# Performance work log

Measured on AMD Instinct MI355X. Metric: run time of the kernel, lower is better.

Reference implementation:

```python
import jax, jax.numpy as jnp
import numpy as np

N = 30000; E = 480000; B = 60
IN = 200; ID = 128; H = 128
NEXP = 4; TOPK = 2; TEMP = 1.5
HEADS = 4; DH = H // HEADS


def _ln(x, g, b):
    mu = jnp.mean(x, -1, keepdims=True)
    var = jnp.var(x, -1, keepdims=True)
    return (x - mu) / jnp.sqrt(var + 1e-5) * g + b


def _seg_sum(d, i, n):
    return jax.ops.segment_sum(d, i, num_segments=n)


def setup_inputs():
    key = jax.random.key(0)
    kit = iter(jax.random.split(key, 80))
    def w(*s):
        return jax.random.normal(next(kit), s, jnp.float32) * 0.05
    inp = {}
    inp['x'] = jax.random.normal(next(kit), (N, IN), jnp.float32)
    inp['node_identity'] = jax.random.normal(next(kit), (N, ID), jnp.float32)
    inp['edge_index'] = jax.random.randint(next(kit), (2, E), 0, N)
    inp['batch'] = jnp.sort(jax.random.randint(next(kit), (N,), 0, B))
    inp.update(fe_W=w(IN, H), fe_b=jnp.zeros(H), fe_g=jnp.ones(H), fe_be=jnp.zeros(H))
    inp.update(ie_W=w(ID, H), ie_b=jnp.zeros(H), ie_g=jnp.ones(H), ie_be=jnp.zeros(H))
    inp.update(fuse_W=w(2 * H, H), fuse_b=jnp.zeros(H), fuse_g=jnp.ones(H), fuse_be=jnp.zeros(H))
    inp.update(router_W=w(2 * H, NEXP))
    inp.update(mlp_W1=w(H, H), mlp_b1=jnp.zeros(H), mlp_W2=w(H, H), mlp_b2=jnp.zeros(H))
    inp.update(cheb_W=w(2, 2, H, H), cheb_b=jnp.zeros((2, H)))
    inp.update(gt_Wq=w(2, H, H), gt_bq=jnp.zeros((2, H)), gt_Wk=w(2, H, H), gt_bk=jnp.zeros((2, H)),
               gt_Wv=w(2, H, H), gt_bv=jnp.zeros((2, H)), gt_Ws=w(2, H, H), gt_bs=jnp.zeros((2, H)))
    inp.update(gcn_W=w(2, H, H), gcn_b=jnp.zeros((2, H)))
    inp.update(pn_g=jnp.ones((NEXP, H)), pn_b=jnp.zeros((NEXP, H)), expert_scales=jnp.ones(NEXP))
    inp.update(h1_W=w(H, H), h1_b=jnp.zeros(H), h1_g=jnp.ones(H), h1_be=jnp.zeros(H))
    inp.update(h2_W=w(H, H // 2), h2_b=jnp.zeros(H // 2), h2_g=jnp.ones(H // 2), h2_be=jnp.zeros(H // 2))
    inp.update(h3_W=w(H // 2, 2), h3_b=jnp.zeros(2), logit_bias=jnp.zeros(2))
    return inp


def _forward(x, node_identity, edge_index, batch, fe_W, fe_b, fe_g, fe_be, ie_W, ie_b, ie_g, ie_be,
             fuse_W, fuse_b, fuse_g, fuse_be, router_W, mlp_W1, mlp_b1, mlp_W2, mlp_b2, cheb_W, cheb_b,
             gt_Wq, gt_bq, gt_Wk, gt_bk, gt_Wv, gt_bv, gt_Ws, gt_bs, gcn_W, gcn_b, pn_g, pn_b,
             expert_scales, h1_W, h1_b, h1_g, h1_be, h2_W, h2_b, h2_g, h2_be, h3_W, h3_b, logit_bias):
    relu = jax.nn.relu
    src, dst = edge_index[0], edge_index[1]
    # encoders + fuse
    h_x = relu(_ln(x @ fe_W + fe_b, fe_g, fe_be))
    h_id = relu(_ln(node_identity @ ie_W + ie_b, ie_g, ie_be))
    h_router = jnp.concatenate([h_x, h_id], -1)
    h = relu(_ln(h_router @ fuse_W + fuse_b, fuse_g, fuse_be))
    # noisy top-k router (eval: no noise, no dropout)
    node_logits = h_router @ router_W
    probs = jax.nn.softmax(node_logits / TEMP, -1)
    vals, idx = jax.lax.top_k(probs, TOPK)
    wts = vals / jnp.clip(jnp.sum(vals, -1, keepdims=True), 1e-9)
    gates = jnp.zeros_like(probs).at[jnp.arange(N)[:, None], idx].set(wts)  # [N, 4]
    # degree / normalization terms
    ones_e = jnp.ones(E, jnp.float32)
    deg = _seg_sum(ones_e, dst, N)
    dinv = jnp.where(deg > 0, jax.lax.rsqrt(jnp.maximum(deg, 1.0)), 0.0)
    dinvl = jax.lax.rsqrt(deg + 1.0)  # with self loops (GCN)
    enorm = dinv[src] * dinv[dst]
    enorml = dinvl[src] * dinvl[dst]
    def aprop(xx, en, di_self=None):
        out = _seg_sum(xx[src] * en[:, None], dst, N)
        if di_self is not None:
            out = out + xx * di_self[:, None]
        return out
    # Expert 0: MLP (2 layers)
    e0 = relu(h @ mlp_W1 + mlp_b1) @ mlp_W2 + mlp_b2
    # Expert 1: ChebNet K=2 (lambda_max=2 -> L_hat = -A_norm), 2 layers
    z = h
    for l in range(2):
        tx1 = -aprop(z, enorm)
        z = z @ cheb_W[l, 0] + tx1 @ cheb_W[l, 1] + cheb_b[l]
        if l == 0:
            z = relu(z)
    e1 = z
    # Expert 2: Graph Transformer, 2 layers, heads=4, root-weight skip
    z = h
    for l in range(2):
        q = (z @ gt_Wq[l] + gt_bq[l]).reshape(N, HEADS, DH)
        k = (z @ gt_Wk[l] + gt_bk[l]).reshape(N, HEADS, DH)
        v = (z @ gt_Wv[l] + gt_bv[l]).reshape(N, HEADS, DH)
        logits = jnp.sum(q[dst] * k[src], -1) * (1.0 / DH ** 0.5)  # [E, heads]
        m = jax.ops.segment_max(logits, dst, num_segments=N)
        m = jnp.where(jnp.isfinite(m), m, 0.0)
        p = jnp.exp(logits - m[dst])
        denom = jnp.clip(_seg_sum(p, dst, N), 1e-9)
        attn = p / denom[dst]
        agg = _seg_sum(attn[:, :, None] * v[src], dst, N).reshape(N, H)
        z = agg + z @ gt_Ws[l] + gt_bs[l]
        if l == 0:
            z = relu(z)
    e2 = z
    # Expert 3: GCN, 2 layers, self loops
    z = h
    for l in range(2):
        zw = z @ gcn_W[l]
        z = aprop(zw, enorml, dinvl * dinvl) + gcn_b[l]
        if l == 0:
            z = relu(z)
    e3 = z
    # per-expert post-norm, scale, gated combine + residual
    eo = jnp.stack([e0, e1, e2, e3], 0)  # [4, N, H]
    eo = _ln(eo, pn_g[:, None, :], pn_b[:, None, :]) * expert_scales[:, None, None]
    out = h + jnp.einsum('ne,enh->nh', gates, eo)
    # mean-pool readout per graph
    counts = jnp.clip(_seg_sum(jnp.ones(N, jnp.float32), batch, B), 1.0)
    pooled = _seg_sum(out, batch, B) / counts[:, None]
    # classification head
    zc = relu(_ln(pooled @ h1_W + h1_b, h1_g, h1_be))
    zc = relu(_ln(zc @ h2_W + h2_b, h2_g, h2_be))
    return zc @ h3_W + h3_b + logit_bias


def reference(x, node_identity, edge_index, batch, fe_W, fe_b, fe_g, fe_be, ie_W, ie_b, ie_g, ie_be,
              fuse_W, fuse_b, fuse_g, fuse_be, router_W, mlp_W1, mlp_b1, mlp_W2, mlp_b2, cheb_W, cheb_b,
              gt_Wq, gt_bq, gt_Wk, gt_bk, gt_Wv, gt_bv, gt_Ws, gt_bs, gcn_W, gcn_b, pn_g, pn_b,
              expert_scales, h1_W, h1_b, h1_g, h1_be, h2_W, h2_b, h2_g, h2_be, h3_W, h3_b, logit_bias):
    return _forward(x, node_identity, edge_index, batch, fe_W, fe_b, fe_g, fe_be, ie_W, ie_b, ie_g, ie_be,
                    fuse_W, fuse_b, fuse_g, fuse_be, router_W, mlp_W1, mlp_b1, mlp_W2, mlp_b2, cheb_W, cheb_b,
                    gt_Wq, gt_bq, gt_Wk, gt_bk, gt_Wv, gt_bv, gt_Ws, gt_bs, gcn_W, gcn_b, pn_g, pn_b,
                    expert_scales, h1_W, h1_b, h1_g, h1_be, h2_W, h2_b, h2_g, h2_be, h3_W, h3_b, logit_bias)
```

## Files before the change

### kernel.cpp

```cpp
#include <hip/hip_runtime.h>

#define RELUF 1
#define ACCF  2
#define LNF   4
#define PCH   32
#define NWT   19
#define SCH   2048

typedef unsigned short ushort_t;
typedef __attribute__((ext_vector_type(8))) short bf16x8;
typedef __attribute__((ext_vector_type(4))) float f32x4;

__device__ __forceinline__ float bf2f(unsigned int v) {
    return __uint_as_float(v << 16);
}
__device__ __forceinline__ unsigned int f2bu(float f) {
    unsigned int u = __float_as_uint(f);
    return (u + 0x7fffu + ((u >> 16) & 1u)) >> 16;
}
__device__ __forceinline__ void unpack8(uint4 u, float* f) {
    f[0] = bf2f(u.x & 0xffff); f[1] = bf2f(u.x >> 16);
    f[2] = bf2f(u.y & 0xffff); f[3] = bf2f(u.y >> 16);
    f[4] = bf2f(u.z & 0xffff); f[5] = bf2f(u.z >> 16);
    f[6] = bf2f(u.w & 0xffff); f[7] = bf2f(u.w >> 16);
// ... 99 lines not shown
        dinvl[i] = rsqrtf(deg + 1.f);
    }
}

struct WtPack {
    const float* src[NWT];
    unsigned long long off[NWT];
    int K[NWT];
};
__global__ void wconv_kernel(WtPack p, ushort_t* __restrict__ base) {
    int a = blockIdx.y;
    const float* s = p.src[a];
    ushort_t* d = base + p.off[a];
    int K = p.K[a];
    int total = K * 128;
    for (int i = blockIdx.x * blockDim.x + threadIdx.x; i < total; i += gridDim.x * blockDim.x) {
        int k = i >> 7, n = i & 127;
        d[n * K + k] = (ushort_t)f2bu(s[i]);
    }
}

__global__ __launch_bounds__(256)
void gemm_f32_ln_kernel(const float* __restrict__ A, int lda, int K,
                        const ushort_t* __restrict__ Wt,
                        ushort_t* __restrict__ Cb,
                        int M,
                        const float* __restrict__ bias,
                        const float* __restrict__ g, const float* __restrict__ be,
                        const float* __restrict__ rW,
                        float* __restrict__ logits)
{
    __shared__ ushort_t As[64][40];
    __shared__ ushort_t Bs[128][40];
    const int tid = threadIdx.x;
    const int m0 = blockIdx.x * 64;
    const int lane = tid & 63;
    const int wv = tid >> 6;
    const int q = lane >> 4;
    const int l16 = lane & 15;
    const int sar = tid >> 2;
    const int sak = (tid & 3) << 3;
    const int sbn = tid >> 1;
    const int sbk = (tid & 1) << 4;
    const bool arow_ok = (m0 + sar) < M;
    const float* Arow = A + (size_t)(m0 + sar) * lda;
    const ushort_t* Wrow = Wt + (size_t)sbn * K;

    f32x4 acc[8];
#pragma unroll
    for (int t = 0; t < 8; t++) acc[t] = (f32x4){0.f, 0.f, 0.f, 0.f};

    for (int k0 = 0; k0 < K; k0 += 32) {
        uint4 apk;
        if (arow_ok && k0 + sak + 8 <= K) {
            float4 p0 = *(const float4*)(Arow + k0 + sak);
            float4 p1 = *(const float4*)(Arow + k0 + sak + 4);
            apk.x = f2bu(p0.x) | (f2bu(p0.y) << 16);
            apk.y = f2bu(p0.z) | (f2bu(p0.w) << 16);
            apk.z = f2bu(p1.x) | (f2bu(p1.y) << 16);
            apk.w = f2bu(p1.z) | (f2bu(p1.w) << 16);
        } else {
            unsigned int t4[4] = {0, 0, 0, 0};
            for (int j = 0; j < 8; j++) {
                int k = k0 + sak + j;
                unsigned int bv = (arow_ok && k < K) ? f2bu(Arow[k]) : 0u;
                t4[j >> 1] |= bv << ((j & 1) * 16);
            }
            apk = make_uint4(t4[0], t4[1], t4[2], t4[3]);
        }
        uint4 b0, b1;
        if (k0 + sbk + 16 <= K) {
            b0 = *(const uint4*)(Wrow + k0 + sbk);
            b1 = *(const uint4*)(Wrow + k0 + sbk + 8);
        } else {
            unsigned int t8[8] = {0, 0, 0, 0, 0, 0, 0, 0};
            for (int j = 0; j < 16; j++) {
                int k = k0 + sbk + j;
                unsigned int bv = (k < K) ? (unsigned int)Wrow[k] : 0u;
                t8[j >> 1] |= bv << ((j & 1) * 16);
            }
            b0 = make_uint4(t8[0], t8[1], t8[2], t8[3]);
            b1 = make_uint4(t8[4], t8[5], t8[6], t8[7]);
        }
        __syncthreads();
        *(uint4*)&As[sar][sak] = apk;
        *(uint4*)&Bs[sbn][sbk] = b0;
        *(uint4*)&Bs[sbn][sbk + 8] = b1;
        __syncthreads();
        bf16x8 af = *(const bf16x8*)&As[16 * wv + l16][q * 8];
#pragma unroll
        for (int t = 0; t < 8; t++) {
            bf16x8 bf = *(const bf16x8*)&Bs[t * 16 + l16][q * 8];
            acc[t] = __builtin_amdgcn_mfma_f32_16x16x32_bf16(af, bf, acc[t], 0, 0, 0);
        }
    }
    const int row_base = m0 + 16 * wv + q * 4;
#pragma unroll
    for (int t = 0; t < 8; t++) {
        float bb = bias[t * 16 + l16];
#pragma unroll
        for (int r = 0; r < 4; r++) acc[t][r] += bb;
    }
    float mean[4], inv[4];
#pragma unroll
    for (int r = 0; r < 4; r++) {
        float s = 0.f, sq = 0.f;
#pragma unroll
        for (int t = 0; t < 8; t++) { float v = acc[t][r]; s += v; sq = fmaf(v, v, sq); }
#pragma unroll
        for (int off = 1; off <= 8; off <<= 1) { s += __shfl_xor(s, off); sq += __shfl_xor(sq, off); }
        mean[r] = s * (1.f / 128.f);
        float var = sq * (1.f / 128.f) - mean[r] * mean[r];
        inv[r] = rsqrtf(var + 1e-5f);
    }
    float rl0[4] = {0, 0, 0, 0}, rl1[4] = {0, 0, 0, 0};
    float rl2[4] = {0, 0, 0, 0}, rl3[4] = {0, 0, 0, 0};
#pragma unroll
    for (int t = 0; t < 8; t++) {
        int col = t * 16 + l16;
        float gg = g[col], b2 = be[col];
        float4 rw = *(const float4*)(rW + col * 4);
#pragma unroll
        for (int r = 0; r < 4; r++) {
            float y = fmaxf(fmaf((acc[t][r] - mean[r]) * inv[r], gg, b2), 0.f);
            rl0[r] = fmaf(y, rw.x, rl0[r]);
            rl1[r] = fmaf(y, rw.y, rl1[r]);
            rl2[r] = fmaf(y, rw.z, rl2[r]);
            rl3[r] = fmaf(y, rw.w, rl3[r]);
            float other = __shfl_xor(y, 1);
            int row = row_base + r;
            if (!(l16 & 1) && row < M) {
                unsigned int pk = f2bu(y) | (f2bu(other) << 16);
                *(unsigned int*)(Cb + (size_t)row * 256 + col) = pk;
            }
        }
    }
#pragma unroll
    for (int r = 0; r < 4; r++) {
#pragma unroll
        for (int off = 1; off <= 8; off <<= 1) {
            rl0[r] += __shfl_xor(rl0[r], off);
            rl1[r] += __shfl_xor(rl1[r], off);
            rl2[r] += __shfl_xor(rl2[r], off);
            rl3[r] += __shfl_xor(rl3[r], off);
        }
        int row = row_base + r;
        if (l16 == 0 && row < M)
            *(float4*)(logits + (size_t)row * 4) = make_float4(rl0[r], rl1[r], rl2[r], rl3[r]);
    }
}

template <int K>
__global__ __launch_bounds__(256)
void gemm_bf_kernel(const ushort_t* __restrict__ A,
                    const ushort_t* __restrict__ Wt,
                    ushort_t* __restrict__ Cb,
                    int M, const float* __restrict__ bias, int flags,
                    const float* __restrict__ g, const float* __restrict__ be)
{
    __shared__ ushort_t As[64][40];
    __shared__ ushort_t Bs[128][40];
    const int tid = threadIdx.x;
    const int m0 = blockIdx.x * 64;
    const int lane = tid & 63;
    const int wv = tid >> 6;
    const int q = lane >> 4;
    const int l16 = lane & 15;
    const int sar = tid >> 2;
    const int sak = (tid & 3) << 3;
    const int sbn = tid >> 1;
    const int sbk = (tid & 1) << 4;
    const bool arow_ok = (m0 + sar) < M;
    const ushort_t* Arow = A + (size_t)(m0 + sar) * K;
    const ushort_t* Wrow = Wt + (size_t)sbn * K;

    f32x4 acc[8];
#pragma unroll
    for (int t = 0; t < 8; t++) acc[t] = (f32x4){0.f, 0.f, 0.f, 0.f};

#pragma unroll
    for (int k0 = 0; k0 < K; k0 += 32) {
        uint4 apk = arow_ok ? *(const uint4*)(Arow + k0 + sak) : make_uint4(0, 0, 0, 0);
        uint4 b0 = *(const uint4*)(Wrow + k0 + sbk);
        uint4 b1 = *(const uint4*)(Wrow + k0 + sbk + 8);
        __syncthreads();
        *(uint4*)&As[sar][sak] = apk;
        *(uint4*)&Bs[sbn][sbk] = b0;
        *(uint4*)&Bs[sbn][sbk + 8] = b1;
        __syncthreads();
        bf16x8 af = *(const bf16x8*)&As[16 * wv + l16][q * 8];
#pragma unroll
        for (int t = 0; t < 8; t++) {
            bf16x8 bf = *(const bf16x8*)&Bs[t * 16 + l16][q * 8];
            acc[t] = __builtin_amdgcn_mfma_f32_16x16x32_bf16(af, bf, acc[t], 0, 0, 0);
        }
    }
    const int row_base = m0 + 16 * wv + q * 4;
    if (flags & LNF) {
#pragma unroll
        for (int t = 0; t < 8; t++) {
            float bb = bias[t * 16 + l16];
#pragma unroll
            for (int r = 0; r < 4; r++) acc[t][r] += bb;
        }
        float mean[4], inv[4];
#pragma unroll
        for (int r = 0; r < 4; r++) {
            float s = 0.f, sq = 0.f;
#pragma unroll
            for (int t = 0; t < 8; t++) { float v = acc[t][r]; s += v; sq = fmaf(v, v, sq); }
#pragma unroll
            for (int off = 1; off <= 8; off <<= 1) { s += __shfl_xor(s, off); sq += __shfl_xor(sq, off); }
            mean[r] = s * (1.f / 128.f);
            float var = sq * (1.f / 128.f) - mean[r] * mean[r];
            inv[r] = rsqrtf(var + 1e-5f);
        }
#pragma unroll
        for (int t = 0; t < 8; t++) {
            int col = t * 16 + l16;
            float gg = g[col], b2 = be[col];
#pragma unroll
            for (int r = 0; r < 4; r++) {
                float y = fmaf((acc[t][r] - mean[r]) * inv[r], gg, b2);
                if (flags & RELUF) y = fmaxf(y, 0.f);
                float other = __shfl_xor(y, 1);
                int row = row_base + r;
                if (!(l16 & 1) && row < M) {
                    unsigned int pk = f2bu(y) | (f2bu(other) << 16);
                    *(unsigned int*)(Cb + (size_t)row * 128 + col) = pk;
                }
            }
        }
        return;
    }
#pragma unroll
    for (int t = 0; t < 8; t++) {
        int col = t * 16 + l16;
        float bb = bias ? bias[col] : 0.f;
#pragma unroll
        for (int r = 0; r < 4; r++) {
            int row = row_base + r;
            bool ok = row < M;
            float val = acc[t][r] + bb;
            if ((flags & ACCF) && ok) val += bf2f(Cb[(size_t)row * 128 + col]);
            if (flags & RELUF) val = fmaxf(val, 0.f);
            float other = __shfl_xor(val, 1);
            if (!(lane & 1) && ok) {
                unsigned int pk = f2bu(val) | (f2bu(other) << 16);
                *(unsigned int*)(Cb + (size_t)row * 128 + col) = pk;
            }
        }
    }
}

__global__ __launch_bounds__(256)
void gemm_dual_kernel(const ushort_t* __restrict__ A1, const ushort_t* __restrict__ Wt1,
                      const ushort_t* __restrict__ A2, const ushort_t* __restrict__ Wt2,
                      ushort_t* __restrict__ Cb, int M,
                      const float* __restrict__ bias, int flags)
{
    const int K = 128;
    __shared__ ushort_t As[64][40];
    __shared__ ushort_t Bs[128][40];
    const int tid = threadIdx.x;
    const int m0 = blockIdx.x * 64;
    const int lane = tid & 63;
    const int wv = tid >> 6;
    const int q = lane >> 4;
    const int l16 = lane & 15;
    const int sar = tid >> 2;
    const int sak = (tid & 3) << 3;
    const int sbn = tid >> 1;
    const int sbk = (tid & 1) << 4;
    const bool arow_ok = (m0 + sar) < M;

    f32x4 acc[8];
#pragma unroll
    for (int t = 0; t < 8; t++) acc[t] = (f32x4){0.f, 0.f, 0.f, 0.f};

    for (int ph = 0; ph < 2; ph++) {
        const ushort_t* Arow = (ph ? A2 : A1) + (size_t)(m0 + sar) * K;
        const ushort_t* Wrow = (ph ? Wt2 : Wt1) + (size_t)sbn * K;
        for (int k0 = 0; k0 < K; k0 += 32) {
            uint4 apk = arow_ok ? *(const uint4*)(Arow + k0 + sak) : make_uint4(0, 0, 0, 0);
            uint4 b0 = *(const uint4*)(Wrow + k0 + sbk);
            uint4 b1 = *(const uint4*)(Wrow + k0 + sbk + 8);
            __syncthreads();
            *(uint4*)&As[sar][sak] = apk;
            *(uint4*)&Bs[sbn][sbk] = b0;
            *(uint4*)&Bs[sbn][sbk + 8] = b1;
            __syncthreads();
            bf16x8 af = *(const bf16x8*)&As[16 * wv + l16][q * 8];
#pragma unroll
            for (int t = 0; t < 8; t++) {
                bf16x8 bf = *(const bf16x8*)&Bs[t * 16 + l16][q * 8];
                acc[t] = __builtin_amdgcn_mfma_f32_16x16x32_bf16(af, bf, acc[t], 0, 0, 0);
            }
        }
    }
#pragma unroll
    for (int t = 0; t < 8; t++) {
        int col = t * 16 + l16;
        float bb = bias ? bias[col] : 0.f;
#pragma unroll
        for (int r = 0; r < 4; r++) {
            int row = m0 + 16 * wv + q * 4 + r;
            bool ok = row < M;
            float val = acc[t][r] + bb;
            if (flags & RELUF) val = fmaxf(val, 0.f);
            float other = __shfl_xor(val, 1);
            if (!(lane & 1) && ok) {
                unsigned int pk = f2bu(val) | (f2bu(other) << 16);
                *(unsigned int*)(Cb + (size_t)row * 128 + col) = pk;
            }
        }
    }
}

__global__ __launch_bounds__(256)
void gemm4_kernel(const ushort_t* __restrict__ A,
                  const ushort_t* __restrict__ Wt,
                  ushort_t* __restrict__ qb,
                  ushort_t* __restrict__ kv,
                  ushort_t* __restrict__ sk,
                  int M,
                  const float* __restrict__ b0, const float* __restrict__ b1,
                  const float* __restrict__ b2, const float* __restrict__ b3)
{
    const int K = 128;
    __shared__ ushort_t As[64][40];
    __shared__ ushort_t Bs[512][40];
    const int tid = threadIdx.x;
    const int m0 = blockIdx.x * 64;
    const int lane = tid & 63;
    const int wv = tid >> 6;
    const int q = lane >> 4;
    const int l16 = lane & 15;
    const int sar = tid >> 2;
    const int sak = (tid & 3) << 3;
    const bool arow_ok = (m0 + sar) < M;
    const ushort_t* Arow = A + (size_t)(m0 + sar) * K;

    f32x4 acc[32];
#pragma unroll
    for (int t = 0; t < 32; t++) acc[t] = (f32x4){0.f, 0.f, 0.f, 0.f};

    for (int k0 = 0; k0 < K; k0 += 32) {
        uint4 apk = arow_ok ? *(const uint4*)(Arow + k0 + sak) : make_uint4(0, 0, 0, 0);
        uint4 bv[4][2];
        int rows[4], kofs[4];
#pragma unroll
        for (int j = 0; j < 4; j++) {
            int slot = tid + j * 256;
            rows[j] = slot >> 1;
            kofs[j] = (slot & 1) << 4;
            const ushort_t* Wrow = Wt + (size_t)rows[j] * K + k0 + kofs[j];
            bv[j][0] = *(const uint4*)Wrow;
            bv[j][1] = *(const uint4*)(Wrow + 8);
        }
        __syncthreads();
        *(uint4*)&As[sar][sak] = apk;
#pragma unroll
        for (int j = 0; j < 4; j++) {
            *(uint4*)&Bs[rows[j]][kofs[j]] = bv[j][0];
            *(uint4*)&Bs[rows[j]][kofs[j] + 8] = bv[j][1];
        }
        __syncthreads();
        bf16x8 af = *(const bf16x8*)&As[16 * wv + l16][q * 8];
#pragma unroll
        for (int t = 0; t < 32; t++) {
            bf16x8 bf = *(const bf16x8*)&Bs[t * 16 + l16][q * 8];
            acc[t] = __builtin_amdgcn_mfma_f32_16x16x32_bf16(af, bf, acc[t], 0, 0, 0);
        }
    }
    const float* bs4[4] = {b0, b1, b2, b3};
#pragma unroll
    for (int s = 0; s < 4; s++) {
#pragma unroll
        for (int t8 = 0; t8 < 8; t8++) {
            int t = s * 8 + t8;
            int col = t8 * 16 + l16;
            float bb = bs4[s][col];
#pragma unroll
            for (int r = 0; r < 4; r++) {
                int row = m0 + 16 * wv + q * 4 + r;
                bool ok = row < M;
                float val = acc[t][r] + bb;
                float other = __shfl_xor(val, 1);
                if (!(lane & 1) && ok) {
                    unsigned int pk = f2bu(val) | (f2bu(other) << 16);
                    if (s == 0)
                        *(unsigned int*)(qb + (size_t)row * 128 + col) = pk;
                    else if (s == 3)
                        *(unsigned int*)(sk + (size_t)row * 128 + col) = pk;
                    else
                        *(unsigned int*)(kv + (size_t)row * 256 + (s - 1) * 128 + col) = pk;
                }
            }
        }
    }
}

__global__ void topk_kernel(const float* __restrict__ la, const float* __restrict__ lb,
                            float* __restrict__ gates, int M)
{
    int n = blockIdx.x * blockDim.x + threadIdx.x;
    if (n >= M) return;
    float4 a = *(const float4*)(la + (size_t)n * 4);
    float4 b = *(const float4*)(lb + (size_t)n * 4);
    float l[4] = {(a.x + b.x) * (1.f / 1.5f), (a.y + b.y) * (1.f / 1.5f),
                  (a.z + b.z) * (1.f / 1.5f), (a.w + b.w) * (1.f / 1.5f)};
    float mx = fmaxf(fmaxf(l[0], l[1]), fmaxf(l[2], l[3]));
    float e[4], ssum = 0.f;
#pragma unroll
    for (int i = 0; i < 4; i++) { e[i] = expf(l[i] - mx); ssum += e[i]; }
    float p[4];
#pragma unroll
    for (int i = 0; i < 4; i++) p[i] = e[i] / ssum;
    int i0 = 0;
    for (int i = 1; i < 4; i++) if (p[i] > p[i0]) i0 = i;
    int i1 = -1;
    for (int i = 0; i < 4; i++) {
        if (i == i0) continue;
        if (i1 < 0 || p[i] > p[i1]) i1 = i;
    }
    float wsum = fmaxf(p[i0] + p[i1], 1e-9f);
    float gg[4] = {0.f, 0.f, 0.f, 0.f};
    gg[i0] = p[i0] / wsum;
    gg[i1] = p[i1] / wsum;
    *(float4*)(gates + (size_t)n * 4) = make_float4(gg[0], gg[1], gg[2], gg[3]);
}

__global__ void edge_deg_kernel(const int* __restrict__ dst, int* __restrict__ degi, int E) {
    int e = blockIdx.x * blockDim.x + threadIdx.x;
    if (e < E) atomicAdd(&degi[dst[e]], 1);
}
__global__ void csr_fill_kernel(const int* __restrict__ src, const int* __restrict__ dst,
                                const int* __restrict__ rowptr, int* __restrict__ cursor,
                                int* __restrict__ csr,
                                const float* __restrict__ dinv, const float* __restrict__ dinvl,
                                float* __restrict__ ecA, float* __restrict__ ecB, int E) {
    int e = blockIdx.x * blockDim.x + threadIdx.x;
    if (e >= E) return;
    int d = dst[e];
    int s = src[e];
    int pos = atomicAdd(&cursor[d], 1);
    int o = rowptr[d] + pos;
    csr[o] = s;
    ecA[o] = dinv[d] * dinv[s];
    ecB[o] = dinvl[d] * dinvl[s];
}

__global__ void gather2_kernel(const ushort_t* __restrict__ Xb,
                               ushort_t* __restrict__ OutA, ushort_t* __restrict__ OutB,
                               const int* __restrict__ rowptr, const int* __restrict__ csr,
                               const float* __restrict__ ecA, const float* __restrict__ ecB,
                               const float* __restrict__ dinvl, int M)
{
    int node = blockIdx.x * 4 + (threadIdx.x >> 6);
    int lane = threadIdx.x & 63;
    if (node >= M) return;
    int beg = rowptr[node], end = rowptr[node + 1];
    int slot = lane >> 4, g = lane & 15;
    float aA[8] = {0, 0, 0, 0, 0, 0, 0, 0};
    float aB[8] = {0, 0, 0, 0, 0, 0, 0, 0};
    int s0 = 0, s1 = 0;
    float cA0 = 0.f, cB0 = 0.f, cA1 = 0.f, cB1 = 0.f;
    {
        int r0 = beg + slot, r1 = beg + 4 + slot;
        if (r0 < end) { s0 = csr[r0]; cA0 = ecA[r0]; cB0 = ecB[r0]; }
        if (r1 < end) { s1 = csr[r1]; cA1 = ecA[r1]; cB1 = ecB[r1]; }
    }
    for (int e = beg; e < end; e += 8) {
        int ns0 = 0, ns1 = 0;
        float nA0 = 0.f, nB0 = 0.f, nA1 = 0.f, nB1 = 0.f;
        int nr0 = e + 8 + slot, nr1 = e + 12 + slot;
        if (nr0 < end) { ns0 = csr[nr0]; nA0 = ecA[nr0]; nB0 = ecB[nr0]; }
        if (nr1 < end) { ns1 = csr[nr1]; nA1 = ecA[nr1]; nB1 = ecB[nr1]; }
        uint4 x0 = *(const uint4*)(Xb + (size_t)s0 * 128 + g * 8);
        uint4 x1 = *(const uint4*)(Xb + (size_t)s1 * 128 + g * 8);
        fma8(x0, cA0, aA); fma8(x0, cB0, aB);
        fma8(x1, cA1, aA); fma8(x1, cB1, aB);
        s0 = ns0; s1 = ns1;
        cA0 = nA0; cB0 = nB0; cA1 = nA1; cB1 = nB1;
    }
#pragma unroll
    for (int j = 0; j < 8; j++) {
        aA[j] += __shfl_xor(aA[j], 16); aA[j] += __shfl_xor(aA[j], 32);
        aB[j] += __shfl_xor(aB[j], 16); aB[j] += __shfl_xor(aB[j], 32);
    }
    {
        float c = dinvl[node]; c *= c;
        uint4 xs = *(const uint4*)(Xb + (size_t)node * 128 + g * 8);
        fma8(xs, c, aB);
    }
    if (lane < 16) {
        float oA[8], oB[8];
#pragma unroll
        for (int j = 0; j < 8; j++) { oA[j] = -aA[j]; oB[j] = aB[j]; }
        size_t ofs = (size_t)node * 128 + g * 8;
        *(uint4*)(OutA + ofs) = pack8(oA);
        *(uint4*)(OutB + ofs) = pack8(oB);
    }
}

__global__ void gather_l2_kernel(const ushort_t* __restrict__ XA, const ushort_t* __restrict__ XB,
                                 ushort_t* __restrict__ OutA, ushort_t* __restrict__ OutB,
                                 const int* __restrict__ rowptr, const int* __restrict__ csr,
                                 const float* __restrict__ ecA, const float* __restrict__ ecB,
                                 const float* __restrict__ dinvl, int M)
{
    int node = blockIdx.x * 4 + (threadIdx.x >> 6);
    int lane = threadIdx.x & 63;
    if (node >= M) return;
    int beg = rowptr[node], end = rowptr[node + 1];
    int slot = lane >> 4, g = lane & 15;
    float aA[8] = {0, 0, 0, 0, 0, 0, 0, 0};
    float aB[8] = {0, 0, 0, 0, 0, 0, 0, 0};
    int s0 = 0, s1 = 0;
    float cA0 = 0.f, cB0 = 0.f, cA1 = 0.f, cB1 = 0.f;
    {
        int r0 = beg + slot, r1 = beg + 4 + slot;
        if (r0 < end) { s0 = csr[r0]; cA0 = ecA[r0]; cB0 = ecB[r0]; }
        if (r1 < end) { s1 = csr[r1]; cA1 = ecA[r1]; cB1 = ecB[r1]; }
    }
    for (int e = beg; e < end; e += 8) {
        int ns0 = 0, ns1 = 0;
        float nA0 = 0.f, nB0 = 0.f, nA1 = 0.f, nB1 = 0.f;
        int nr0 = e + 8 + slot, nr1 = e + 12 + slot;
        if (nr0 < end) { ns0 = csr[nr0]; nA0 = ecA[nr0]; nB0 = ecB[nr0]; }
        if (nr1 < end) { ns1 = csr[nr1]; nA1 = ecA[nr1]; nB1 = ecB[nr1]; }
        uint4 a0 = *(const uint4*)(XA + (size_t)s0 * 128 + g * 8);
        uint4 a1 = *(const uint4*)(XA + (size_t)s1 * 128 + g * 8);
        uint4 b0 = *(const uint4*)(XB + (size_t)s0 * 128 + g * 8);
        uint4 b1 = *(const uint4*)(XB + (size_t)s1 * 128 + g * 8);
        fma8(a0, cA0, aA); fma8(a1, cA1, aA);
        fma8(b0, cB0, aB); fma8(b1, cB1, aB);
        s0 = ns0; s1 = ns1;
        cA0 = nA0; cB0 = nB0; cA1 = nA1; cB1 = nB1;
    }
#pragma unroll
    for (int j = 0; j < 8; j++) {
        aA[j] += __shfl_xor(aA[j], 16); aA[j] += __shfl_xor(aA[j], 32);
        aB[j] += __shfl_xor(aB[j], 16); aB[j] += __shfl_xor(aB[j], 32);
    }
    {
        float c = dinvl[node]; c *= c;
        uint4 xs = *(const uint4*)(XB + (size_t)node * 128 + g * 8);
        fma8(xs, c, aB);
    }
// ... 88 lines not shown
        ba[ee] = pnb[ee * 128 + lane * 2];
        bb[ee] = pnb[ee * 128 + lane * 2 + 1];
        es[ee] = esc[ee];
    }
    float sx = 0.f, sy = 0.f;
    for (int n = s0 + c; n < e0i; n += PCH) {
        size_t ofs = (size_t)n * 128 + lane * 2;
        float4 gg = *(const float4*)(gates + (size_t)n * 4);
        float gv[4] = {gg.x, gg.y, gg.z, gg.w};
        unsigned int hu = *(const unsigned int*)(hb + ofs);
        float ox = bf2f(hu & 0xffff), oy = bf2f(hu >> 16);
#pragma unroll
        for (int ee = 0; ee < 4; ee++) {
            unsigned int u = *(const unsigned int*)(eps[ee] + ofs);
            float vx = bf2f(u & 0xffff), vy = bf2f(u >> 16);
            float su = vx + vy, sq = vx * vx + vy * vy;
#pragma unroll
            for (int off = 32; off; off >>= 1) { su += __shfl_xor(su, off); sq += __shfl_xor(sq, off); }
            float mean = su * (1.f / 128.f);
            float var = sq * (1.f / 128.f) - mean * mean;
            float inv = rsqrtf(var + 1e-5f);
            float cc = es[ee] * gv[ee];
            ox = fmaf(cc, (vx - mean) * inv * ga[ee] + ba[ee], ox);
            oy = fmaf(cc, (vy - mean) * inv * gb[ee] + bb[ee], oy);
        }
        sx += ox; sy += oy;
    }
    *(float2*)(partial + ((size_t)b * PCH + c) * 128 + lane * 2) = make_float2(sx, sy);
}

__global__ void head_kernel(const float* __restrict__ partial,
                            const int* __restrict__ bstart, const int* __restrict__ bend,
                            const float* __restrict__ h1W, const float* __restrict__ h1b,
                            const float* __restrict__ h1g, const float* __restrict__ h1be,
                            const float* __restrict__ h2W, const float* __restrict__ h2b,
                            const float* __restrict__ h2g, const float* __restrict__ h2be,
                            const float* __restrict__ h3W, const float* __restrict__ h3b,
                            const float* __restrict__ lbias,
                            float* __restrict__ out, int B)
{
    __shared__ float p[128], z[128];
    int b = blockIdx.x, t = threadIdx.x;
    float sum = 0.f;
#pragma unroll
    for (int c = 0; c < PCH; c++) sum += partial[((size_t)b * PCH + c) * 128 + t];
    float cnt = fmaxf((float)(bend[b] - bstart[b]), 1.f);
    p[t] = sum / cnt;
    __syncthreads();
    float a = h1b[t];
    for (int k = 0; k < 128; k++) a = fmaf(p[k], h1W[k * 128 + t], a);
    z[t] = a;
    __syncthreads();
    float s = 0.f, sq = 0.f;
    for (int k = 0; k < 128; k++) { float x = z[k]; s += x; sq += x * x; }
    float mean = s * (1.f / 128.f), var = sq * (1.f / 128.f) - mean * mean;
    float y = fmaxf((a - mean) * rsqrtf(var + 1e-5f) * h1g[t] + h1be[t], 0.f);
    __syncthreads();
    z[t] = y;
    __syncthreads();
    float a2 = 0.f;
    if (t < 64) {
        a2 = h2b[t];
        for (int k = 0; k < 128; k++) a2 = fmaf(z[k], h2W[k * 64 + t], a2);
    }
    __syncthreads();
    if (t < 64) p[t] = a2;
    __syncthreads();
    if (t < 2) {
        float s2 = 0.f, sq2 = 0.f;
        for (int k = 0; k < 64; k++) { float x = p[k]; s2 += x; sq2 += x * x; }
        float mean2 = s2 * (1.f / 64.f), var2 = sq2 * (1.f / 64.f) - mean2 * mean2;
        float inv2 = rsqrtf(var2 + 1e-5f);
        float o = h3b[t] + lbias[t];
        for (int k = 0; k < 64; k++) {
            float zc = fmaxf((p[k] - mean2) * inv2 * h2g[k] + h2be[k], 0.f);
            o = fmaf(zc, h3W[k * 2 + t], o);
        }
        out[b * 2 + t] = o;
    }
}

extern "C" void kernel_launch(void* const* d_in, const int* in_sizes, int n_in,
                              void* d_out, int out_size, void* d_ws, size_t ws_size,
                              hipStream_t stream)
{
    (void)ws_size; (void)n_in;
    const int N = in_sizes[3];
    const int E = in_sizes[2] / 2;
    const int B = out_size / 2;

    const int* ei = (const int*)d_in[2];
    const int* src = ei;
    const int* dst = ei + E;
    const int* batch = (const int*)d_in[3];

    const float* W[47];
    for (int i = 0; i < 47; i++) W[i] = (const float*)d_in[i];

    size_t fN = (size_t)N;
    float* gates   = (float*)d_ws;
    float* dinv    = gates + 4 * fN;
    float* dinvl   = dinv + fN;
    float* partial = dinvl + fN;
    float* logitsA = partial + (size_t)128 * B * PCH;
    float* logitsB = logitsA + 4 * fN;
    ushort_t* hb  = (ushort_t*)(logitsB + 4 * fN);
    ushort_t* e0b = hb + 128 * fN;
    ushort_t* e1b = e0b + 128 * fN;
    ushort_t* e2b = e1b + 128 * fN;
    ushort_t* e3b = e2b + 128 * fN;
    ushort_t* x0  = e3b + 128 * fN;
    ushort_t* x1  = x0 + 128 * fN;
    ushort_t* x2  = x1 + 128 * fN;
    ushort_t* x3  = x2 + 128 * fN;
    ushort_t* qb  = x3 + 128 * fN;
    ushort_t* kvb = qb + 128 * fN;
    ushort_t* hrb = kvb + 256 * fN;
    ushort_t* wt  = hrb + 256 * fN;
    WtPack wp;
    const float* wsrc[NWT] = {
        W[4], W[8], W[12], W[17], W[19],
        W[21], W[21] + 16384, W[21] + 32768, W[21] + 49152,
        W[23], W[25], W[27], W[29],
        W[23] + 16384, W[25] + 16384, W[27] + 16384, W[29] + 16384,
        W[31], W[31] + 16384
    };
    const int wk[NWT] = {200, 128, 256, 128, 128,
                         128, 128, 128, 128,
                         128, 128, 128, 128,
                         128, 128, 128, 128,
                         128, 128};
    unsigned long long woff[NWT];
    unsigned long long acc_off = 0;
    for (int i = 0; i < NWT; i++) {
        wp.src[i] = wsrc[i];
        wp.K[i] = wk[i];
        wp.off[i] = acc_off;
        woff[i] = acc_off;
        acc_off += (unsigned long long)128 * wk[i];
    }
    int* degi   = (int*)(wt + acc_off + 8);
    int* cursor = degi + N;
    int* rowptr = cursor + N;
    int* csr    = rowptr + (N + 1);
    int* bstart = csr + E;
    int* bend   = bstart + B;
    int* bsum   = bend + B;
    float* ecA  = (float*)(bsum + 256);
    float* ecB  = ecA + E;

    dim3 blk(256);
    int gN4 = (N + 3) / 4;
    dim3 gG((N + 63) / 64);
    int nsb = (N + SCH - 1) / SCH;

    wconv_kernel<<<dim3(32, NWT), blk, 0, stream>>>(wp, wt);
    zero2_kernel<<<(2 * N + 255) / 256, blk, 0, stream>>>(degi, 2 * N, bstart, 2 * B);
    seg_bounds_kernel<<<(N + 255) / 256, blk, 0, stream>>>(batch, bstart, bend, N);
    edge_deg_kernel<<<(E + 255) / 256, blk, 0, stream>>>(dst, degi, E);
    scan1_kernel<<<dim3(nsb), blk, 0, stream>>>(degi, rowptr, bsum, N);
    scan2_kernel<<<1, blk, 0, stream>>>(bsum, nsb);
    scan3_kernel<<<(N + 255) / 256, blk, 0, stream>>>(rowptr, bsum, degi, dinv, dinvl, N);
    csr_fill_kernel<<<(E + 255) / 256, blk, 0, stream>>>(src, dst, rowptr, cursor, csr,
                                                         dinv, dinvl, ecA, ecB, E);

    gemm_f32_ln_kernel<<<gG, blk, 0, stream>>>(W[0], 200, 200, wt + woff[0], hrb, N,
                                               W[5], W[6], W[7], W[16], logitsA);
    gemm_f32_ln_kernel<<<gG, blk, 0, stream>>>(W[1], 128, 128, wt + woff[1], hrb + 128, N,
                                               W[9], W[10], W[11], W[16] + 512, logitsB);
    topk_kernel<<<(N + 255) / 256, blk, 0, stream>>>(logitsA, logitsB, gates, N);
    gemm_bf_kernel<256><<<gG, blk, 0, stream>>>(hrb, wt + woff[2], hb, N,
                                                W[13], RELUF | LNF, W[14], W[15]);

    gemm_bf_kernel<128><<<gG, blk, 0, stream>>>(hb, wt + woff[3], x0, N, W[18], RELUF, 0, 0);
    gemm_bf_kernel<128><<<gG, blk, 0, stream>>>(x0, wt + woff[4], e0b, N, W[20], 0, 0, 0);

    gather2_kernel<<<gN4, blk, 0, stream>>>(hb, x1, x2, rowptr, csr, ecA, ecB, dinvl, N);

    gemm_dual_kernel<<<gG, blk, 0, stream>>>(hb, wt + woff[5], x1, wt + woff[6],
                                             x0, N, W[22], RELUF);
    gemm_bf_kernel<128><<<gG, blk, 0, stream>>>(x2, wt + woff[17], x1, N, W[32], RELUF, 0, 0);

    gather_l2_kernel<<<gN4, blk, 0, stream>>>(x0, x1, x3, x2, rowptr, csr, ecA, ecB, dinvl, N);

    gemm_dual_kernel<<<gG, blk, 0, stream>>>(x0, wt + woff[7], x3, wt + woff[8],
                                             e1b, N, W[22] + 128, 0);
    gemm_bf_kernel<128><<<gG, blk, 0, stream>>>(x2, wt + woff[18], e3b, N, W[32] + 128, 0, 0, 0);

    gemm4_kernel<<<gG, blk, 0, stream>>>(hb, wt + woff[9], qb, kvb, x3, N,
                                         W[24], W[26], W[28], W[30]);
    gt_attn_kernel<<<gN4, blk, 0, stream>>>(qb, kvb, rowptr, csr, x3, 1, x1, N);
    gemm4_kernel<<<gG, blk, 0, stream>>>(x1, wt + woff[13], qb, kvb, x3, N,
                                         W[24] + 128, W[26] + 128, W[28] + 128, W[30] + 128);
    gt_attn_kernel<<<gN4, blk, 0, stream>>>(qb, kvb, rowptr, csr, x3, 0, e2b, N);

    pool_combine_kernel<<<dim3(B, PCH), dim3(64), 0, stream>>>(
        hb, e0b, e1b, e2b, e3b, gates, W[33], W[34], W[35], bstart, bend, partial);
    head_kernel<<<dim3(B), dim3(128), 0, stream>>>(partial, bstart, bend,
        W[36], W[37], W[38], W[39],
        W[40], W[41], W[42], W[43],
        W[44], W[45], W[46],
        (float*)d_out, B);
}
```

Measured before the change: 580.5 us.

## Replace LDS-tiled bf16 GEMMs with per-wave register GEMMs reading global memory

After: 641.9 us. +10.6%, slower.

```diff
diff --git a/kernel.cpp b/kernel.cpp
--- a/kernel.cpp
+++ b/kernel.cpp
@@ -275,100 +275,45 @@
 
 template <int K>
 __global__ __launch_bounds__(256)
-void gemm_bf_kernel(const ushort_t* __restrict__ A,
+void gemm_wv_kernel(const ushort_t* __restrict__ A,
                     const ushort_t* __restrict__ Wt,
-                    ushort_t* __restrict__ Cb,
-                    int M, const float* __restrict__ bias, int flags,
-                    const float* __restrict__ g, const float* __restrict__ be)
-{
-    __shared__ ushort_t As[64][40];
-    __shared__ ushort_t Bs[128][40];
-    const int tid = threadIdx.x;
-    const int m0 = blockIdx.x * 64;
-    const int lane = tid & 63;
-    const int wv = tid >> 6;
-    const int q = lane >> 4;
-    const int l16 = lane & 15;
-    const int sar = tid >> 2;
-    const int sak = (tid & 3) << 3;
-    const int sbn = tid >> 1;
-    const int sbk = (tid & 1) << 4;
-    const bool arow_ok = (m0 + sar) < M;
-    const ushort_t* Arow = A + (size_t)(m0 + sar) * K;
-    const ushort_t* Wrow = Wt + (size_t)sbn * K;
-
-    f32x4 acc[8];
-#pragma unroll
-    for (int t = 0; t < 8; t++) acc[t] = (f32x4){0.f, 0.f, 0.f, 0.f};
-
+                    ushort_t* __restrict__ Cb, int M,
+                    const float* __restrict__ bias, int relu)
+{
+    int w = blockIdx.x * 4 + (threadIdx.x >> 6);
+    int lane = threadIdx.x & 63;
+    int ct = w & 3;
+    int rt = w >> 2;
+    int row0 = rt * 16;
+    if (row0 >= M) return;
+    int l16 = lane & 15, q = lane >> 4;
+    int arow = row0 + l16;
+    bool aok = arow < M;
+    const ushort_t* Ar = A + (size_t)arow * K + q * 8;
+    const ushort_t* W0 = Wt + (size_t)(ct * 32 + l16) * K + q * 8;
+    const ushort_t* W1 = W0 + (size_t)16 * K;
+    bf16x8 zz = {0, 0, 0, 0, 0, 0, 0, 0};
+    f32x4 a0 = {0.f, 0.f, 0.f, 0.f}, a1 = {0.f, 0.f, 0.f, 0.f};
 #pragma unroll
     for (int k0 = 0; k0 < K; k0 += 32) {
-        uint4 apk = arow_ok ? *(const uint4*)(Arow + k0 + sak) : make_uint4(0, 0, 0, 0);
-        uint4 b0 = *(const uint4*)(Wrow + k0 + sbk);
-        uint4 b1 = *(const uint4*)(Wrow + k0 + sbk + 8);
-        __syncthreads();
-        *(uint4*)&As[sar][sak] = apk;
-        *(uint4*)&Bs[sbn][sbk] = b0;
-        *(uint4*)&Bs[sbn][sbk + 8] = b1;
-        __syncthreads();
-        bf16x8 af = *(const bf16x8*)&As[16 * wv + l16][q * 8];
-#pragma unroll
-        for (int t = 0; t < 8; t++) {
-            bf16x8 bf = *(const bf16x8*)&Bs[t * 16 + l16][q * 8];
-            acc[t] = __builtin_amdgcn_mfma_f32_16x16x32_bf16(af, bf, acc[t], 0, 0, 0);
-        }
-    }
-    const int row_base = m0 + 16 * wv + q * 4;
-    if (flags & LNF) {
-#pragma unroll
-        for (int t = 0; t < 8; t++) {
-            float bb = bias[t * 16 + l16];
-#pragma unroll
-            for (int r = 0; r < 4; r++) acc[t][r] += bb;
-        }
-        float mean[4], inv[4];
+        bf16x8 af = aok ? *(const bf16x8*)(Ar + k0) : zz;
+        bf16x8 b0 = *(const bf16x8*)(W0 + k0);
+        bf16x8 b1 = *(const bf16x8*)(W1 + k0);
+        a0 = __builtin_amdgcn_mfma_f32_16x16x32_bf16(af, b0, a0, 0, 0, 0);
+        a1 = __builtin_amdgcn_mfma_f32_16x16x32_bf16(af, b1, a1, 0, 0, 0);
+    }
+    f32x4 av[2] = {a0, a1};
+#pragma unroll
+    for (int t = 0; t < 2; t++) {
+        int col = ct * 32 + t * 16 + l16;
+        float bb = bias ? bias[col] : 0.f;
 #pragma unroll
         for (int r = 0; r < 4; r++) {
-            float s = 0.f, sq = 0.f;
-#pragma unroll
-            for (int t = 0; t < 8; t++) { float v = acc[t][r]; s += v; sq = fmaf(v, v, sq); }
-#pragma unroll
-            for (int off = 1; off <= 8; off <<= 1) { s += __shfl_xor(s, off); sq += __shfl_xor(sq, off); }
-            mean[r] = s * (1.f / 128.f);
-            float var = sq * (1.f / 128.f) - mean[r] * mean[r];
-            inv[r] = rsqrtf(var + 1e-5f);
-        }
-#pragma unroll
-        for (int t = 0; t < 8; t++) {
-            int col = t * 16 + l16;
-            float gg = g[col], b2 = be[col];
-#pragma unroll
-            for (int r = 0; r < 4; r++) {
-                float y = fmaf((acc[t][r] - mean[r]) * inv[r], gg, b2);
-                if (flags & RELUF) y = fmaxf(y, 0.f);
-                float other = __shfl_xor(y, 1);
-                int row = row_base + r;
-                if (!(l16 & 1) && row < M) {
-                    unsigned int pk = f2bu(y) | (f2bu(other) << 16);
-                    *(unsigned int*)(Cb + (size_t)row * 128 + col) = pk;
-                }
-            }
-        }
-        return;
-    }
-#pragma unroll
-    for (int t = 0; t < 8; t++) {
-        int col = t * 16 + l16;
-        float bb = bias ? bias[col] : 0.f;
-#pragma unroll
-        for (int r = 0; r < 4; r++) {
-            int row = row_base + r;
-            bool ok = row < M;
-            float val = acc[t][r] + bb;
-            if ((flags & ACCF) && ok) val += bf2f(Cb[(size_t)row * 128 + col]);
-            if (flags & RELUF) val = fmaxf(val, 0.f);
+            int row = row0 + q * 4 + r;
+            float val = av[t][r] + bb;
+            if (relu) val = fmaxf(val, 0.f);
             float other = __shfl_xor(val, 1);
-            if (!(lane & 1) && ok) {
+            if (!(l16 & 1) && row < M) {
                 unsigned int pk = f2bu(val) | (f2bu(other) << 16);
                 *(unsigned int*)(Cb + (size_t)row * 128 + col) = pk;
             }
@@ -377,62 +322,51 @@
 }
 
 __global__ __launch_bounds__(256)
-void gemm_dual_kernel(const ushort_t* __restrict__ A1, const ushort_t* __restrict__ Wt1,
-                      const ushort_t* __restrict__ A2, const ushort_t* __restrict__ Wt2,
-                      ushort_t* __restrict__ Cb, int M,
-                      const float* __restrict__ bias, int flags)
+void gemm_dual_wv_kernel(const ushort_t* __restrict__ A1, const ushort_t* __restrict__ Wt1,
+                         const ushort_t* __restrict__ A2, const ushort_t* __restrict__ Wt2,
+                         ushort_t* __restrict__ Cb, int M,
+                         const float* __restrict__ bias, int relu)
 {
     const int K = 128;
-    __shared__ ushort_t As[64][40];
-    __shared__ ushort_t Bs[128][40];
-    const int tid = threadIdx.x;
-    const int m0 = blockIdx.x * 64;
-    const int lane = tid & 63;
-    const int wv = tid >> 6;
-    const int q = lane >> 4;
-    const int l16 = lane & 15;
-    const int sar = tid >> 2;
-    const int sak = (tid & 3) << 3;
-    const int sbn = tid >> 1;
-    const int sbk = (tid & 1) << 4;
-    const bool arow_ok = (m0 + sar) < M;
-
-    f32x4 acc[8];
-#pragma unroll
-    for (int t = 0; t < 8; t++) acc[t] = (f32x4){0.f, 0.f, 0.f, 0.f};
-
+    int w = blockIdx.x * 4 + (threadIdx.x >> 6);
+    int lane = threadIdx.x & 63;
+    int ct = w & 3;
+    int rt = w >> 2;
+    int row0 = rt * 16;
+    if (row0 >= M) return;
+    int l16 = lane & 15, q = lane >> 4;
+    int arow = row0 + l16;
+    bool aok = arow < M;
+    size_t aofs = (size_t)arow * K + q * 8;
+    size_t wofs = (size_t)(ct * 32 + l16) * K + q * 8;
+    bf16x8 zz = {0, 0, 0, 0, 0, 0, 0, 0};
+    f32x4 a0 = {0.f, 0.f, 0.f, 0.f}, a1 = {0.f, 0.f, 0.f, 0.f};
+#pragma unroll
     for (int ph = 0; ph < 2; ph++) {
-        const ushort_t* Arow = (ph ? A2 : A1) + (size_t)(m0 + sar) * K;
-        const ushort_t* Wrow = (ph ? Wt2 : Wt1) + (size_t)sbn * K;
+        const ushort_t* Ar = (ph ? A2 : A1) + aofs;
+        const ushort_t* W0 = (ph ? Wt2 : Wt1) + wofs;
+        const ushort_t* W1 = W0 + (size_t)16 * K;
+#pragma unroll
         for (int k0 = 0; k0 < K; k0 += 32) {
-            uint4 apk = arow_ok ? *(const uint4*)(Arow + k0 + sak) : make_uint4(0, 0, 0, 0);
-            uint4 b0 = *(const uint4*)(Wrow + k0 + sbk);
-            uint4 b1 = *(const uint4*)(Wrow + k0 + sbk + 8);
-            __syncthreads();
-            *(uint4*)&As[sar][sak] = apk;
-            *(uint4*)&Bs[sbn][sbk] = b0;
-            *(uint4*)&Bs[sbn][sbk + 8] = b1;
-            __syncthreads();
-            bf16x8 af = *(const bf16x8*)&As[16 * wv + l16][q * 8];
-#pragma unroll
-            for (int t = 0; t < 8; t++) {
-                bf16x8 bf = *(const bf16x8*)&Bs[t * 16 + l16][q * 8];
-                acc[t] = __builtin_amdgcn_mfma_f32_16x16x32_bf16(af, bf, acc[t], 0, 0, 0);
-            }
-        }
-    }
-#pragma unroll
-    for (int t = 0; t < 8; t++) {
-        int col = t * 16 + l16;
+            bf16x8 af = aok ? *(const bf16x8*)(Ar + k0) : zz;
+            bf16x8 b0 = *(const bf16x8*)(W0 + k0);
+            bf16x8 b1 = *(const bf16x8*)(W1 + k0);
+            a0 = __builtin_amdgcn_mfma_f32_16x16x32_bf16(af, b0, a0, 0, 0, 0);
+            a1 = __builtin_amdgcn_mfma_f32_16x16x32_bf16(af, b1, a1, 0, 0, 0);
+        }
+    }
+    f32x4 av[2] = {a0, a1};
+#pragma unroll
+    for (int t = 0; t < 2; t++) {
+        int col = ct * 32 + t * 16 + l16;
         float bb = bias ? bias[col] : 0.f;
 #pragma unroll
         for (int r = 0; r < 4; r++) {
-            int row = m0 + 16 * wv + q * 4 + r;
-            bool ok = row < M;
-            float val = acc[t][r] + bb;
-            if (flags & RELUF) val = fmaxf(val, 0.f);
+            int row = row0 + q * 4 + r;
+            float val = av[t][r] + bb;
+            if (relu) val = fmaxf(val, 0.f);
             float other = __shfl_xor(val, 1);
-            if (!(lane & 1) && ok) {
+            if (!(l16 & 1) && row < M) {
                 unsigned int pk = f2bu(val) | (f2bu(other) << 16);
                 *(unsigned int*)(Cb + (size_t)row * 128 + col) = pk;
             }
@@ -441,84 +375,123 @@
 }
 
 __global__ __launch_bounds__(256)
-void gemm4_kernel(const ushort_t* __restrict__ A,
-                  const ushort_t* __restrict__ Wt,
-                  ushort_t* __restrict__ qb,
-                  ushort_t* __restrict__ kv,
-                  ushort_t* __restrict__ sk,
-                  int M,
-                  const float* __restrict__ b0, const float* __restrict__ b1,
-                  const float* __restrict__ b2, const float* __restrict__ b3)
+void gemm4_wv_kernel(const ushort_t* __restrict__ A,
+                     const ushort_t* __restrict__ Wt,
+                     ushort_t* __restrict__ qb, ushort_t* __restrict__ kv,
+                     ushort_t* __restrict__ sk, int M,
+                     const float* __restrict__ b0, const float* __restrict__ b1,
+                     const float* __restrict__ b2, const float* __restrict__ b3)
 {
     const int K = 128;
-    __shared__ ushort_t As[64][40];
-    __shared__ ushort_t Bs[512][40];
-    const int tid = threadIdx.x;
-    const int m0 = blockIdx.x * 64;
-    const int lane = tid & 63;
-    const int wv = tid >> 6;
-    const int q = lane >> 4;
-    const int l16 = lane & 15;
-    const int sar = tid >> 2;
-    const int sak = (tid & 3) << 3;
-    const bool arow_ok = (m0 + sar) < M;
-    const ushort_t* Arow = A + (size_t)(m0 + sar) * K;
-
-    f32x4 acc[32];
-#pragma unroll
-    for (int t = 0; t < 32; t++) acc[t] = (f32x4){0.f, 0.f, 0.f, 0.f};
-
+    int w = blockIdx.x * 4 + (threadIdx.x >> 6);
+    int lane = threadIdx.x & 63;
+    int ct = w & 15;
+    int rt = w >> 4;
+    int row0 = rt * 16;
+    if (row0 >= M) return;
+    int l16 = lane & 15, q = lane >> 4;
+    int arow = row0 + l16;
+    bool aok = arow < M;
+    const ushort_t* Ar = A + (size_t)arow * K + q * 8;
+    const ushort_t* W0 = Wt + (size_t)(ct * 32 + l16) * K + q * 8;
+    const ushort_t* W1 = W0 + (size_t)16 * K;
+    bf16x8 zz = {0, 0, 0, 0, 0, 0, 0, 0};
+    f32x4 a0 = {0.f, 0.f, 0.f, 0.f}, a1 = {0.f, 0.f, 0.f, 0.f};
+#pragma unroll
     for (int k0 = 0; k0 < K; k0 += 32) {
-        uint4 apk = arow_ok ? *(const uint4*)(Arow + k0 + sak) : make_uint4(0, 0, 0, 0);
-        uint4 bv[4][2];
-        int rows[4], kofs[4];
-#pragma unroll
-        for (int j = 0; j < 4; j++) {
-            int slot = tid + j * 256;
-            rows[j] = slot >> 1;
-            kofs[j] = (slot & 1) << 4;
-            const ushort_t* Wrow = Wt + (size_t)rows[j] * K + k0 + kofs[j];
-            bv[j][0] = *(const uint4*)Wrow;
-            bv[j][1] = *(const uint4*)(Wrow + 8);
-        }
-        __syncthreads();
-        *(uint4*)&As[sar][sak] = apk;
-#pragma unroll
-        for (int j = 0; j < 4; j++) {
-            *(uint4*)&Bs[rows[j]][kofs[j]] = bv[j][0];
-            *(uint4*)&Bs[rows[j]][kofs[j] + 8] = bv[j][1];
-        }
-        __syncthreads();
-        bf16x8 af = *(const bf16x8*)&As[16 * wv + l16][q * 8];
-#pragma unroll
-        for (int t = 0; t < 32; t++) {
-            bf16x8 bf = *(const bf16x8*)&Bs[t * 16 + l16][q * 8];
+        bf16x8 af = aok ? *(const bf16x8*)(Ar + k0) : zz;
+        bf16x8 bb0 = *(const bf16x8*)(W0 + k0);
+        bf16x8 bb1 = *(const bf16x8*)(W1 + k0);
+        a0 = __builtin_amdgcn_mfma_f32_16x16x32_bf16(af, bb0, a0, 0, 0, 0);
+        a1 = __builtin_amdgcn_mfma_f32_16x16x32_bf16(af, bb1, a1, 0, 0, 0);
+    }
+    int s = ct >> 2, ct2 = ct & 3;
+    const float* bs4[4] = {b0, b1, b2, b3};
+    const float* bs = bs4[s];
+    ushort_t* dstp;
+    int stride;
+    if (s == 0) { dstp = qb; stride = 128; }
+    else if (s == 3) { dstp = sk; stride = 128; }
+    else { dstp = kv + (s - 1) * 128; stride = 256; }
+    f32x4 av[2] = {a0, a1};
+#pragma unroll
+    for (int t = 0; t < 2; t++) {
+        int col = ct2 * 32 + t * 16 + l16;
+        float bb = bs[ct2 * 32 + t * 16 + l16];
+#pragma unroll
+        for (int r = 0; r < 4; r++) {
+            int row = row0 + q * 4 + r;
+            float val = av[t][r] + bb;
+            float other = __shfl_xor(val, 1);
+            if (!(l16 & 1) && row < M) {
+                unsigned int pk = f2bu(val) | (f2bu(other) << 16);
+                *(unsigned int*)(dstp + (size_t)row * stride + col) = pk;
+            }
+        }
+    }
+}
+
+template <int K>
+__global__ __launch_bounds__(256)
+void gemm_ln_wv_kernel(const ushort_t* __restrict__ A,
+                       const ushort_t* __restrict__ Wt,
+                       ushort_t* __restrict__ Cb, int M,
+                       const float* __restrict__ bias,
+                       const float* __restrict__ g, const float* __restrict__ be, int relu)
+{
+    int w = blockIdx.x * 4 + (threadIdx.x >> 6);
+    int lane = threadIdx.x & 63;
+    int row0 = w * 16;
+    if (row0 >= M) return;
+    int l16 = lane & 15, q = lane >> 4;
+    int arow = row0 + l16;
+    bool aok = arow < M;
+    const ushort_t* Ar = A + (size_t)arow * K + q * 8;
+    const ushort_t* Wr = Wt + (size_t)l16 * K + q * 8;
+    bf16x8 zz = {0, 0, 0, 0, 0, 0, 0, 0};
+    f32x4 acc[8];
+#pragma unroll
+    for (int t = 0; t < 8; t++) acc[t] = (f32x4){0.f, 0.f, 0.f, 0.f};
+#pragma unroll
+    for (int k0 = 0; k0 < K; k0 += 32) {
+        bf16x8 af = aok ? *(const bf16x8*)(Ar + k0) : zz;
+#pragma unroll
+        for (int t = 0; t < 8; t++) {
+            bf16x8 bf = *(const bf16x8*)(Wr + (size_t)t * 16 * K + k0);
             acc[t] = __builtin_amdgcn_mfma_f32_16x16x32_bf16(af, bf, acc[t], 0, 0, 0);
         }
     }
-    const float* bs4[4] = {b0, b1, b2, b3};
-#pragma unroll
-    for (int s = 0; s < 4; s++) {
-#pragma unroll
-        for (int t8 = 0; t8 < 8; t8++) {
-            int t = s * 8 + t8;
-            int col = t8 * 16 + l16;
-            float bb = bs4[s][col];
-#pragma unroll
-            for (int r = 0; r < 4; r++) {
-                int row = m0 + 16 * wv + q * 4 + r;
-                bool ok = row < M;
-                float val = acc[t][r] + bb;
-                float other = __shfl_xor(val, 1);
-                if (!(lane & 1) && ok) {
-                    unsigned int pk = f2bu(val) | (f2bu(other) << 16);
-                    if (s == 0)
-                        *(unsigned int*)(qb + (size_t)row * 128 + col) = pk;
-                    else if (s == 3)
-                        *(unsigned int*)(sk + (size_t)row * 128 + col) = pk;
-                    else
-                        *(unsigned int*)(kv + (size_t)row * 256 + (s - 1) * 128 + col) = pk;
-                }
+#pragma unroll
+    for (int t = 0; t < 8; t++) {
+        float bb = bias[t * 16 + l16];
+#pragma unroll
+        for (int r = 0; r < 4; r++) acc[t][r] += bb;
+    }
+    float mean[4], inv[4];
+#pragma unroll
+    for (int r = 0; r < 4; r++) {
+        float s = 0.f, sq = 0.f;
+#pragma unroll
+        for (int t = 0; t < 8; t++) { float v = acc[t][r]; s += v; sq = fmaf(v, v, sq); }
+#pragma unroll
+        for (int off = 1; off <= 8; off <<= 1) { s += __shfl_xor(s, off); sq += __shfl_xor(sq, off); }
+        mean[r] = s * (1.f / 128.f);
+        float var = sq * (1.f / 128.f) - mean[r] * mean[r];
+        inv[r] = rsqrtf(var + 1e-5f);
+    }
+#pragma unroll
+    for (int t = 0; t < 8; t++) {
+        int col = t * 16 + l16;
+        float gg = g[col], b2 = be[col];
+#pragma unroll
+        for (int r = 0; r < 4; r++) {
+            float y = fmaf((acc[t][r] - mean[r]) * inv[r], gg, b2);
+            if (relu) y = fmaxf(y, 0.f);
+            float other = __shfl_xor(y, 1);
+            int row = row0 + q * 4 + r;
+            if (!(l16 & 1) && row < M) {
+                unsigned int pk = f2bu(y) | (f2bu(other) << 16);
+                *(unsigned int*)(Cb + (size_t)row * 128 + col) = pk;
             }
         }
     }
@@ -913,6 +886,7 @@
     dim3 blk(256);
     int gN4 = (N + 3) / 4;
     dim3 gG((N + 63) / 64);
+    int RT = (N + 15) / 16;
     int nsb = (N + SCH - 1) / SCH;
 
     wconv_kernel<<<dim3(32, NWT), blk, 0, stream>>>(wp, wt);
@@ -930,29 +904,29 @@
     gemm_f32_ln_kernel<<<gG, blk, 0, stream>>>(W[1], 128, 128, wt + woff[1], hrb + 128, N,
                                                W[9], W[10], W[11], W[16] + 512, logitsB);
     topk_kernel<<<(N + 255) / 256, blk, 0, stream>>>(logitsA, logitsB, gates, N);
-    gemm_bf_kernel<256><<<gG, blk, 0, stream>>>(hrb, wt + woff[2], hb, N,
-                                                W[13], RELUF | LNF, W[14], W[15]);
-
-    gemm_bf_kernel<128><<<gG, blk, 0, stream>>>(hb, wt + woff[3], x0, N, W[18], RELUF, 0, 0);
-    gemm_bf_kernel<128><<<gG, blk, 0, stream>>>(x0, wt + woff[4], e0b, N, W[20], 0, 0, 0);
+    gemm_ln_wv_kernel<256><<<(RT + 3) / 4, blk, 0, stream>>>(hrb, wt + woff[2], hb, N,
+                                                             W[13], W[14], W[15], 1);
+
+    gemm_wv_kernel<128><<<RT, blk, 0, stream>>>(hb, wt + woff[3], x0, N, W[18], 1);
+    gemm_wv_kernel<128><<<RT, blk, 0, stream>>>(x0, wt + woff[4], e0b, N, W[20], 0);
 
     gather2_kernel<<<gN4, blk, 0, stream>>>(hb, x1, x2, rowptr, csr, ecA, ecB, dinvl, N);
 
-    gemm_dual_kernel<<<gG, blk, 0, stream>>>(hb, wt + woff[5], x1, wt + woff[6],
-                                             x0, N, W[22], RELUF);
-    gemm_bf_kernel<128><<<gG, blk, 0, stream>>>(x2, wt + woff[17], x1, N, W[32], RELUF, 0, 0);
+    gemm_dual_wv_kernel<<<RT, blk, 0, stream>>>(hb, wt + woff[5], x1, wt + woff[6],
+                                                x0, N, W[22], 1);
+    gemm_wv_kernel<128><<<RT, blk, 0, stream>>>(x2, wt + woff[17], x1, N, W[32], 1);
 
     gather_l2_kernel<<<gN4, blk, 0, stream>>>(x0, x1, x3, x2, rowptr, csr, ecA, ecB, dinvl, N);
 
-    gemm_dual_kernel<<<gG, blk, 0, stream>>>(x0, wt + woff[7], x3, wt + woff[8],
-                                             e1b, N, W[22] + 128, 0);
-    gemm_bf_kernel<128><<<gG, blk, 0, stream>>>(x2, wt + woff[18], e3b, N, W[32] + 128, 0, 0, 0);
-
-    gemm4_kernel<<<gG, blk, 0, stream>>>(hb, wt + woff[9], qb, kvb, x3, N,
-                                         W[24], W[26], W[28], W[30]);
+    gemm_dual_wv_kernel<<<RT, blk, 0, stream>>>(x0, wt + woff[7], x3, wt + woff[8],
+                                                e1b, N, W[22] + 128, 0);
+    gemm_wv_kernel<128><<<RT, blk, 0, stream>>>(x2, wt + woff[18], e3b, N, W[32] + 128, 0);
+
+    gemm4_wv_kernel<<<RT * 4, blk, 0, stream>>>(hb, wt + woff[9], qb, kvb, x3, N,
+                                                W[24], W[26], W[28], W[30]);
     gt_attn_kernel<<<gN4, blk, 0, stream>>>(qb, kvb, rowptr, csr, x3, 1, x1, N);
-    gemm4_kernel<<<gG, blk, 0, stream>>>(x1, wt + woff[13], qb, kvb, x3, N,
-                                         W[24] + 128, W[26] + 128, W[28] + 128, W[30] + 128);
+    gemm4_wv_kernel<<<RT * 4, blk, 0, stream>>>(x1, wt + woff[13], qb, kvb, x3, N,
+                                                W[24] + 128, W[26] + 128, W[28] + 128, W[30] + 128);
     gt_attn_kernel<<<gN4, blk, 0, stream>>>(qb, kvb, rowptr, csr, x3, 0, e2b, N);
 
     pool_combine_kernel<<<dim3(B, PCH), dim3(64), 0, stream>>>(
```
